# Performance work log

Measured on AMD Instinct MI355X. Metric: run time of the kernel, lower is better.

## Reference

```python
import jax, jax.numpy as jnp
import numpy as np

VOCAB = 32000
HIDDEN = 256
BATCH = 32
SEQ = 128


def setup_inputs() -> dict:
    key = jax.random.key(0)
    ks = jax.random.split(key, 9)
    stdv = 1.0 / np.sqrt(HIDDEN)
    tokens = jax.random.randint(ks[0], (BATCH, SEQ), 0, VOCAB)
    lengths = jax.random.randint(ks[1], (BATCH,), 1, SEQ + 1)
    emb = jax.random.normal(ks[2], (VOCAB, HIDDEN), dtype=jnp.float32)
    W_x1 = jax.random.uniform(ks[3], (HIDDEN, HIDDEN), jnp.float32, -stdv, stdv)
    W_h1 = jax.random.uniform(ks[4], (HIDDEN, HIDDEN), jnp.float32, -stdv, stdv)
    b1 = jnp.zeros((HIDDEN,), jnp.float32)
    W_x2 = jax.random.uniform(ks[5], (HIDDEN, HIDDEN), jnp.float32, -stdv, stdv)
    W_h2 = jax.random.uniform(ks[6], (HIDDEN, HIDDEN), jnp.float32, -stdv, stdv)
    b2 = jnp.zeros((HIDDEN,), jnp.float32)
    return {"tokens": tokens, "lengths": lengths, "emb": emb,
            "W_x1": W_x1, "W_h1": W_h1, "b1": b1,
            "W_x2": W_x2, "W_h2": W_h2, "b2": b2}


def _rnn_layer(x, W_x, W_h, b, mask):
    # x: [B,T,H] (already zeroed at padded positions, matching pad_packed_sequence)
    B = x.shape[0]
    h0 = jnp.zeros((B, W_h.shape[0]), x.dtype)

    def step(h, x_t):
        # torch: tanh(W_x @ x_t[...,None] + W_h @ h[...,None]).squeeze() + b)
        h = jnp.tanh(x_t @ W_x.T + h @ W_h.T + b)
        return h, h

    _, hs = jax.lax.scan(step, h0, jnp.swapaxes(x, 0, 1))  # [T,B,H]
    hs = jnp.swapaxes(hs, 0, 1)  # [B,T,H]
    # pack_padded_sequence drops padded steps -> zero them out
    return hs * mask[:, :, None]


def reference(tokens, lengths, emb, W_x1, W_h1, b1, W_x2, W_h2, b2):
    B, T = tokens.shape
    mask = (jnp.arange(T)[None, :] < lengths[:, None]).astype(emb.dtype)  # [B,T]
    # Model.forward: argmax of one-hot -> token ids -> embedding lookup
    x = emb[tokens] * mask[:, :, None]  # [B,T,H], padded positions are zeros
    h1 = _rnn_layer(x, W_x1, W_h1, b1, mask)
    h2 = _rnn_layer(h1, W_x2, W_h2, b2, mask)
    logits = h2 @ emb.T  # [B,T,V] tied output projection
    probs = jax.nn.softmax(logits, axis=-1) * mask[:, :, None]
    return probs, h2
```

## Files before the change

kernel.cpp:

```cpp
#include <hip/hip_runtime.h>
#include <hip/hip_bf16.h>

#define VOCAB 32000
#define HID   256
#define BATCH 32
#define SEQ   128
#define MROWS (BATCH * SEQ)
#define NCB   250

typedef _Float16 f16;
typedef _Float16 f16x4 __attribute__((ext_vector_type(4)));
typedef _Float16 f16x8 __attribute__((ext_vector_type(8)));
typedef float    f32x4 __attribute__((ext_vector_type(4)));

#define GLOAD_LDS16(gptr, lptr)                                                       \
  __builtin_amdgcn_global_load_lds(                                                   \
      (const __attribute__((address_space(1))) unsigned int*)(gptr),                  \
      (__attribute__((address_space(3))) unsigned int*)(lptr), 16, 0, 0)

__global__ __launch_bounds__(256) void embed_kernel(
    const int* __restrict__ tokens, const int* __restrict__ lengths,
    const float* __restrict__ emb, float* __restrict__ x) {
  int row = blockIdx.x;
  int b = row >> 7, t = row & 127;
  int tok = tokens[row];
  float v = (t < lengths[b]) ? emb[(size_t)tok * HID + threadIdx.x] : 0.f;
  x[(size_t)row * HID + threadIdx.x] = v;
}

__global__ __launch_bounds__(256) void cast_kernel(
    const float* __restrict__ in, f16* __restrict__ out, int n4) {
  int idx = blockIdx.x * 256 + threadIdx.x;
  if (idx >= n4) return;
  float4 v = ((const float4*)in)[idx];
  f16x4 o = {(f16)v.x, (f16)v.y, (f16)v.z, (f16)v.w};
  ((f16x4*)out)[idx] = o;
}

__global__ __launch_bounds__(256) void xprep_kernel(
    const float* __restrict__ In, const float* __restrict__ W,
    const float* __restrict__ bias, float* __restrict__ Out) {
  __shared__ float sIn[16 * 256];
  int tid = threadIdx.x;
  int rb = blockIdx.x * 16;
  const float4* g = (const float4*)(In + (size_t)rb * 256);
  float4* s4 = (float4*)sIn;
#pragma unroll
  for (int q = 0; q < 4; ++q) s4[tid + q * 256] = g[tid + q * 256];
  __syncthreads();
  int i = tid;
  float acc[16];
#pragma unroll
  for (int r = 0; r < 16; ++r) acc[r] = 0.f;
  const float4* w4 = (const float4*)(W + (size_t)i * 256);
#pragma unroll 4
  for (int j = 0; j < 64; ++j) {
    float4 wv = w4[j];
#pragma unroll
    for (int r = 0; r < 16; ++r) {
      float4 sv = ((const float4*)(sIn + r * 256))[j];
      acc[r] += sv.x * wv.x + sv.y * wv.y + sv.z * wv.z + sv.w * wv.w;
    }
  }
  float bi = bias[i];
#pragma unroll
  for (int r = 0; r < 16; ++r) Out[(size_t)(rb + r) * 256 + i] = acc[r] + bi;
}

__global__ __launch_bounds__(512) void rnn_kernel(
    const float* __restrict__ X, const float* __restrict__ Wh,
    const int* __restrict__ lengths, float* __restrict__ Hout) {
  int b = blockIdx.x;
  int tid = threadIdx.x;
  int i = tid & 255;
  int half = tid >> 8;
  float w[128];
  {
    const float4* wr = (const float4*)(Wh + (size_t)i * 256 + half * 128);
#pragma unroll
    for (int q = 0; q < 32; ++q) {
      float4 v = wr[q];
      w[4 * q + 0] = v.x; w[4 * q + 1] = v.y;
      w[4 * q + 2] = v.z; w[4 * q + 3] = v.w;
    }
  }
  __shared__ float sh[256];
  __shared__ float sp[256];
  if (tid < 256) sh[tid] = 0.f;
  int len = lengths[b];
  const float* Xb = X + (size_t)b * SEQ * HID;
  float* Hb = Hout + (size_t)b * SEQ * HID;
  __syncthreads();
  float xnext = (half == 0) ? Xb[i] : 0.f;
  for (int t = 0; t < SEQ; ++t) {
    float a0 = 0.f, a1 = 0.f, a2 = 0.f, a3 = 0.f;
    const float4* hp = (const float4*)(sh + half * 128);
#pragma unroll
    for (int q = 0; q < 32; ++q) {
      float4 hv = hp[q];
      a0 += hv.x * w[4 * q + 0];
      a1 += hv.y * w[4 * q + 1];
      a2 += hv.z * w[4 * q + 2];
      a3 += hv.w * w[4 * q + 3];
    }
    float acc = (a0 + a1) + (a2 + a3);
    if (half) sp[i] = acc;
    __syncthreads();
    if (!half) {
      float h = tanhf(xnext + acc + sp[i]);
      Hb[(size_t)t * HID + i] = (t < len) ? h : 0.f;
      sh[i] = h;
      if (t + 1 < SEQ) xnext = Xb[(size_t)(t + 1) * HID + i];
    }
    __syncthreads();
  }
}

template <int WRITE_PROBS>
__global__ __launch_bounds__(256) void gemm_kernel(
    const f16* __restrict__ A,
    const f16* __restrict__ Bm,
    float* __restrict__ C,
    float* __restrict__ PM,
    float* __restrict__ PL,
    const float* __restrict__ Mrow,
    const float* __restrict__ Inv,
    const int* __restrict__ lengths) {
  __shared__ __align__(16) f16 sAbuf[2][128 * 64];
  __shared__ __align__(16) f16 sBbuf[2][128 * 64];
  const int tid = threadIdx.x;
  const int wave = tid >> 6;
  const int lane = tid & 63;

  const int flat = blockIdx.x + 32 * blockIdx.y;
  const int work = (flat & 7) * 1000 + (flat >> 3);
  const int bx = work & 31;
  const int by = work >> 5;
  const int row0 = bx * 128;
  const int col0 = by * 128;

  const int len = lengths[bx];
  const int lenc = (len + 15) & ~15;

  f32x4 acc[4][4];
#pragma unroll
  for (int a = 0; a < 4; ++a)
#pragma unroll
    for (int b = 0; b < 4; ++b) acc[a][b] = (f32x4){0.f, 0.f, 0.f, 0.f};

  const int lr = lane >> 3;
  const int ls = lane & 7;
  const int wm = wave & 1, wn = wave >> 1;

#define STAGE(buf, koo)                                                        \
  {                                                                            \
    _Pragma("unroll") for (int ii = 0; ii < 4; ++ii) {                         \
      int ar = wave * 32 + ii * 8;                                             \
      int r = ar + lr;                                                         \
      int c = ls ^ (r & 7);                                                    \
      if (ar < lenc) {                                                         \
        const f16* ga = A + (size_t)(row0 + r) * 256 + (koo) * 64 + c * 8;     \
        GLOAD_LDS16(ga, sAbuf[buf] + ar * 64);                                 \
      }                                                                        \
      const f16* gb = Bm + (size_t)(col0 + r) * 256 + (koo) * 64 + c * 8;      \
      GLOAD_LDS16(gb, sBbuf[buf] + ar * 64);                                   \
    }                                                                          \
  }

  STAGE(0, 0);
  __syncthreads();

#pragma unroll
  for (int ko = 0; ko < 4; ++ko) {
    const int cur = ko & 1;
    if (ko < 3) STAGE(cur ^ 1, ko + 1);
#pragma unroll
    for (int kk = 0; kk < 2; ++kk) {
      const int cA = kk * 4 + (lane >> 4);
      f16x8 bf[4];
#pragma unroll
      for (int f = 0; f < 4; ++f) {
        int n = wn * 64 + f * 16 + (lane & 15);
        bf[f] = *(const f16x8*)(sBbuf[cur] + n * 64 + (cA ^ (n & 7)) * 8);
      }
#pragma unroll
      for (int fm = 0; fm < 4; ++fm) {
        const int g = fm * 2 + wm;
        if (g * 16 < len) {
          int m = g * 16 + (lane & 15);
          f16x8 af = *(const f16x8*)(sAbuf[cur] + m * 64 + (cA ^ (m & 7)) * 8);
#pragma unroll
          for (int fn = 0; fn < 4; ++fn)
            acc[fm][fn] = __builtin_amdgcn_mfma_f32_16x16x32_f16(
                af, bf[fn], acc[fm][fn], 0, 0, 0);
        }
      }
    }
    __syncthreads();
  }
#undef STAGE

  const int lq = lane >> 4;
  const int lc = lane & 15;

  if (WRITE_PROBS) {
    float* sM = (float*)sAbuf;
    float* sI = sM + 128;
    if (tid < 128) {
      sM[tid] = Mrow[row0 + tid];
      sI[tid] = Inv[row0 + tid];
    }
    __syncthreads();
#pragma unroll
    for (int fm = 0; fm < 4; ++fm)
#pragma unroll
      for (int fn = 0; fn < 4; ++fn)
#pragma unroll
        for (int rr = 0; rr < 4; ++rr) {
          int t = (fm * 2 + wm) * 16 + lq * 4 + rr;
          int col = col0 + wn * 64 + fn * 16 + lc;
          float v =
              (t < len) ? __expf(acc[fm][fn][rr] - sM[t]) * sI[t] : 0.f;
          C[(size_t)(row0 + t) * VOCAB + col] = v;
        }
  } else {
    float* rm = (float*)sAbuf;
    float* rs = rm + 256;
#pragma unroll
    for (int fm = 0; fm < 4; ++fm) {
      const int g = fm * 2 + wm;
      const bool active = (g * 16 < len);
#pragma unroll
      for (int rr = 0; rr < 4; ++rr) {
        int r = g * 16 + lq * 4 + rr;
        if (active) {
          float mx = fmaxf(fmaxf(acc[fm][0][rr], acc[fm][1][rr]),
                           fmaxf(acc[fm][2][rr], acc[fm][3][rr]));
#pragma unroll
          for (int off = 1; off < 16; off <<= 1)
            mx = fmaxf(mx, __shfl_xor(mx, off, 64));
          float sum = __expf(acc[fm][0][rr] - mx) +
                      __expf(acc[fm][1][rr] - mx) +
                      __expf(acc[fm][2][rr] - mx) +
                      __expf(acc[fm][3][rr] - mx);
#pragma unroll
          for (int off = 1; off < 16; off <<= 1)
            sum += __shfl_xor(sum, off, 64);
          if (lc == 0) {
            rm[wn * 128 + r] = mx;
            rs[wn * 128 + r] = sum;
          }
        } else if (lc == 0) {
          rm[wn * 128 + r] = 0.f;
          rs[wn * 128 + r] = 0.f;
        }
      }
    }
    __syncthreads();
    if (tid < 128) {
      float m0 = rm[tid], m1 = rm[128 + tid];
      float M = fmaxf(m0, m1);
      float L = rs[tid] * __expf(m0 - M) + rs[128 + tid] * __expf(m1 - M);
      PM[(size_t)(row0 + tid) * NCB + by] = M;
      PL[(size_t)(row0 + tid) * NCB + by] = L;
    }
  }
}

__global__ __launch_bounds__(256) void combine_kernel(
    const float* __restrict__ PM, const float* __restrict__ PL,
    float* __restrict__ Mrow, float* __restrict__ Inv) {
  int row = blockIdx.x * 4 + (threadIdx.x >> 6);
  int lane = threadIdx.x & 63;
  const float* pm = PM + (size_t)row * NCB;
  const float* pl = PL + (size_t)row * NCB;
  float M = -3.4e38f;
  for (int i = lane; i < NCB; i += 64) M = fmaxf(M, pm[i]);
#pragma unroll
  for (int off = 1; off < 64; off <<= 1) M = fmaxf(M, __shfl_xor(M, off, 64));
  float L = 0.f;
  for (int i = lane; i < NCB; i += 64) L += pl[i] * __expf(pm[i] - M);
#pragma unroll
  for (int off = 1; off < 64; off <<= 1) L += __shfl_xor(L, off, 64);
  if (lane == 0) {
    Mrow[row] = M;
    Inv[row] = 1.f / L;
  }
}

extern "C" void kernel_launch(void* const* d_in, const int* in_sizes, int n_in,
                              void* d_out, int out_size, void* d_ws,
                              size_t ws_size, hipStream_t stream) {
  const int* tokens = (const int*)d_in[0];
  const int* lengths = (const int*)d_in[1];
  const float* emb = (const float*)d_in[2];
  const float* Wx1 = (const float*)d_in[3];
  const float* Wh1 = (const float*)d_in[4];
  const float* b1 = (const float*)d_in[5];
  const float* Wx2 = (const float*)d_in[6];
  const float* Wh2 = (const float*)d_in[7];
  const float* b2 = (const float*)d_in[8];

  float* probs = (float*)d_out;
  float* h2out = probs + (size_t)MROWS * VOCAB;

  float* ws = (float*)d_ws;
  float* x = ws;
  float* X = ws + 1048576;
  float* h1 = ws + 2097152;
  f16* embh = (f16*)(ws + 3145728);
  f16* h2h = (f16*)(ws + 3145728 + 4096000);
  float* PM = ws + 7766016;
  float* PL = ws + 8790016;
  float* Mrow = ws + 9814016;
  float* Inv = ws + 9818112;

  embed_kernel<<<MROWS, 256, 0, stream>>>(tokens, lengths, emb, x);
  cast_kernel<<<8000, 256, 0, stream>>>(emb, embh, VOCAB * HID / 4);

  xprep_kernel<<<256, 256, 0, stream>>>(x, Wx1, b1, X);
  rnn_kernel<<<BATCH, 512, 0, stream>>>(X, Wh1, lengths, h1);
  xprep_kernel<<<256, 256, 0, stream>>>(h1, Wx2, b2, X);
  rnn_kernel<<<BATCH, 512, 0, stream>>>(X, Wh2, lengths, h2out);

  cast_kernel<<<1024, 256, 0, stream>>>(h2out, h2h, MROWS * HID / 4);

  dim3 gg(32, NCB);
  gemm_kernel<0><<<gg, 256, 0, stream>>>(h2h, embh, nullptr, PM, PL,
                                         nullptr, nullptr, lengths);
  combine_kernel<<<MROWS / 4, 256, 0, stream>>>(PM, PL, Mrow, Inv);
  gemm_kernel<1><<<gg, 256, 0, stream>>>(h2h, embh, probs, nullptr, nullptr,
                                         Mrow, Inv, lengths);
}
```

Measured before the change: 1.070 ms.

## Fuse embedding gather and h2 cast into neighbours; restructure RNN reduction

Folds the embedding gather and masking into the first xprep kernel and drops the separate embed launch and its intermediate buffer. The RNN kernel now splits each output's dot product across the two halves of one wave and combines them with a cross-lane shuffle. This, plus a double-buffered hidden state, leaves one barrier per step instead of two. tanh is computed with __expf, and the second RNN writes the fp16 copy of h2 directly, removing a cast kernel. Probability stores become nontemporal. The risks are small accuracy differences from the fast tanh and scattered gather loads inside xprep.

```diff
diff --git a/kernel.cpp b/kernel.cpp
--- a/kernel.cpp
+++ b/kernel.cpp
@@ -17,16 +17,6 @@
   __builtin_amdgcn_global_load_lds(                                                   \
       (const __attribute__((address_space(1))) unsigned int*)(gptr),                  \
       (__attribute__((address_space(3))) unsigned int*)(lptr), 16, 0, 0)
-
-__global__ __launch_bounds__(256) void embed_kernel(
-    const int* __restrict__ tokens, const int* __restrict__ lengths,
-    const float* __restrict__ emb, float* __restrict__ x) {
-  int row = blockIdx.x;
-  int b = row >> 7, t = row & 127;
-  int tok = tokens[row];
-  float v = (t < lengths[b]) ? emb[(size_t)tok * HID + threadIdx.x] : 0.f;
-  x[(size_t)row * HID + threadIdx.x] = v;
-}
 
 __global__ __launch_bounds__(256) void cast_kernel(
     const float* __restrict__ in, f16* __restrict__ out, int n4) {
@@ -37,16 +27,36 @@
   ((f16x4*)out)[idx] = o;
 }
 
+template <int GATHER>
 __global__ __launch_bounds__(256) void xprep_kernel(
-    const float* __restrict__ In, const float* __restrict__ W,
-    const float* __restrict__ bias, float* __restrict__ Out) {
+    const float* __restrict__ In, const int* __restrict__ tokens,
+    const int* __restrict__ lengths, const float* __restrict__ emb,
+    const float* __restrict__ W, const float* __restrict__ bias,
+    float* __restrict__ Out) {
   __shared__ float sIn[16 * 256];
   int tid = threadIdx.x;
   int rb = blockIdx.x * 16;
-  const float4* g = (const float4*)(In + (size_t)rb * 256);
   float4* s4 = (float4*)sIn;
 #pragma unroll
-  for (int q = 0; q < 4; ++q) s4[tid + q * 256] = g[tid + q * 256];
+  for (int q = 0; q < 4; ++q) {
+    int f = tid + q * 256;
+    float4 v;
+    if (GATHER) {
+      int row = f >> 6;
+      int c4 = f & 63;
+      int gr = rb + row;
+      int bb = gr >> 7, t = gr & 127;
+      if (t < lengths[bb]) {
+        int tok = tokens[gr];
+        v = ((const float4*)(emb + (size_t)tok * 256))[c4];
+      } else {
+        v = make_float4(0.f, 0.f, 0.f, 0.f);
+      }
+    } else {
+      v = ((const float4*)(In + (size_t)rb * 256))[f];
+    }
+    s4[f] = v;
+  }
   __syncthreads();
   int i = tid;
   float acc[16];
@@ -69,14 +79,17 @@
 
 __global__ __launch_bounds__(512) void rnn_kernel(
     const float* __restrict__ X, const float* __restrict__ Wh,
-    const int* __restrict__ lengths, float* __restrict__ Hout) {
+    const int* __restrict__ lengths, float* __restrict__ Hout,
+    f16* __restrict__ H16) {
   int b = blockIdx.x;
   int tid = threadIdx.x;
-  int i = tid & 255;
-  int half = tid >> 8;
+  int wave = tid >> 6;
+  int lane = tid & 63;
+  int o = wave * 32 + (lane & 31);
+  int kh = lane >> 5;
   float w[128];
   {
-    const float4* wr = (const float4*)(Wh + (size_t)i * 256 + half * 128);
+    const float4* wr = (const float4*)(Wh + (size_t)o * 256 + kh * 128);
 #pragma unroll
     for (int q = 0; q < 32; ++q) {
       float4 v = wr[q];
@@ -84,17 +97,18 @@
       w[4 * q + 2] = v.z; w[4 * q + 3] = v.w;
     }
   }
-  __shared__ float sh[256];
-  __shared__ float sp[256];
-  if (tid < 256) sh[tid] = 0.f;
+  __shared__ float sh[2][256];
+  if (tid < 256) sh[0][tid] = 0.f;
   int len = lengths[b];
   const float* Xb = X + (size_t)b * SEQ * HID;
   float* Hb = Hout + (size_t)b * SEQ * HID;
+  f16* H16b = H16 + (size_t)b * SEQ * HID;
   __syncthreads();
-  float xnext = (half == 0) ? Xb[i] : 0.f;
+  float xnext = (kh == 0) ? Xb[o] : 0.f;
   for (int t = 0; t < SEQ; ++t) {
+    const int cur = t & 1;
     float a0 = 0.f, a1 = 0.f, a2 = 0.f, a3 = 0.f;
-    const float4* hp = (const float4*)(sh + half * 128);
+    const float4* hp = (const float4*)(sh[cur] + kh * 128);
 #pragma unroll
     for (int q = 0; q < 32; ++q) {
       float4 hv = hp[q];
@@ -104,13 +118,16 @@
       a3 += hv.w * w[4 * q + 3];
     }
     float acc = (a0 + a1) + (a2 + a3);
-    if (half) sp[i] = acc;
-    __syncthreads();
-    if (!half) {
-      float h = tanhf(xnext + acc + sp[i]);
-      Hb[(size_t)t * HID + i] = (t < len) ? h : 0.f;
-      sh[i] = h;
-      if (t + 1 < SEQ) xnext = Xb[(size_t)(t + 1) * HID + i];
+    acc += __shfl_xor(acc, 32, 64);
+    if (kh == 0) {
+      float z = xnext + acc;
+      float e = __expf(2.f * z);
+      float h = 1.f - 2.f / (e + 1.f);
+      float hm = (t < len) ? h : 0.f;
+      Hb[(size_t)t * HID + o] = hm;
+      if (H16) H16b[(size_t)t * HID + o] = (f16)hm;
+      sh[cur ^ 1][o] = h;
+      if (t + 1 < SEQ) xnext = Xb[(size_t)(t + 1) * HID + o];
     }
     __syncthreads();
   }
@@ -221,7 +238,7 @@
           int col = col0 + wn * 64 + fn * 16 + lc;
           float v =
               (t < len) ? __expf(acc[fm][fn][rr] - sM[t]) * sI[t] : 0.f;
-          C[(size_t)(row0 + t) * VOCAB + col] = v;
+          __builtin_nontemporal_store(v, &C[(size_t)(row0 + t) * VOCAB + col]);
         }
   } else {
     float* rm = (float*)sAbuf;
@@ -305,7 +322,6 @@
   float* h2out = probs + (size_t)MROWS * VOCAB;
 
   float* ws = (float*)d_ws;
-  float* x = ws;
   float* X = ws + 1048576;
   float* h1 = ws + 2097152;
   f16* embh = (f16*)(ws + 3145728);
@@ -315,15 +331,14 @@
   float* Mrow = ws + 9814016;
   float* Inv = ws + 9818112;
 
-  embed_kernel<<<MROWS, 256, 0, stream>>>(tokens, lengths, emb, x);
   cast_kernel<<<8000, 256, 0, stream>>>(emb, embh, VOCAB * HID / 4);
 
-  xprep_kernel<<<256, 256, 0, stream>>>(x, Wx1, b1, X);
-  rnn_kernel<<<BATCH, 512, 0, stream>>>(X, Wh1, lengths, h1);
-  xprep_kernel<<<256, 256, 0, stream>>>(h1, Wx2, b2, X);
-  rnn_kernel<<<BATCH, 512, 0, stream>>>(X, Wh2, lengths, h2out);
-
-  cast_kernel<<<1024, 256, 0, stream>>>(h2out, h2h, MROWS * HID / 4);
+  xprep_kernel<1><<<256, 256, 0, stream>>>(nullptr, tokens, lengths, emb,
+                                           Wx1, b1, X);
+  rnn_kernel<<<BATCH, 512, 0, stream>>>(X, Wh1, lengths, h1, nullptr);
+  xprep_kernel<0><<<256, 256, 0, stream>>>(h1, nullptr, nullptr, nullptr,
+                                           Wx2, b2, X);
+  rnn_kernel<<<BATCH, 512, 0, stream>>>(X, Wh2, lengths, h2out, h2h);
 
   dim3 gg(32, NCB);
   gemm_kernel<0><<<gg, 256, 0, stream>>>(h2h, embh, nullptr, PM, PL,
```

Result: no change. 1.056 ms (-1.3%).
